# Optimization experiments

Hardware: AMD Instinct MI355X
Metric: run time of the kernel (lower is better)

## Reference

```python
import jax, jax.numpy as jnp
import numpy as np

C_CLIP = 10.0


def setup_inputs() -> dict:
    key = jax.random.key(0)
    ks = jax.random.split(key, 5)
    B, S, E, H = 128, 2048, 512, 512
    query = jax.random.normal(ks[0], (B, E), dtype=jnp.float32)
    target = jax.random.normal(ks[1], (B, S, E), dtype=jnp.float32)
    mask = jax.random.randint(ks[2], (B, S), 0, 2, dtype=jnp.int32)
    # torch.nn.Linear weights: [out, in], applied as x @ W.T + b
    Wq = jax.random.normal(ks[3], (H, E), dtype=jnp.float32) / np.sqrt(E)
    bq = jnp.zeros((H,), dtype=jnp.float32)
    Wk = jax.random.normal(ks[4], (H, E), dtype=jnp.float32) / np.sqrt(E)
    bk = jnp.zeros((H,), dtype=jnp.float32)
    return {"query": query, "target": target, "mask": mask,
            "Wq": Wq, "bq": bq, "Wk": Wk, "bk": bk}


def reference(query, target, mask, Wq, bq, Wk, bk):
    # q = W_q(query): [B, H]; k = W_k(target): [B, S, H]
    q = query @ Wq.T + bq
    k = jnp.einsum('bse,he->bsh', target, Wk) + bk
    # score qk[b,s] = sum_h q[b,h] * k[b,s,h]
    qk = jnp.einsum('bh,bsh->bs', q, k)
    qk = C_CLIP * jnp.tanh(qk)
    qk = jnp.where(mask == 1, -jnp.inf, qk)
    alpha = jax.nn.softmax(qk, axis=-1)
    return alpha
```

## Files before the change

### kernel.cpp

```cpp
#include <hip/hip_runtime.h>
#include <math.h>

#define Bsz 128
#define Ssz 2048
#define Esz 512
#define Hsz 512
#define C_CLIPF 10.0f
#define CHUNK 128

__device__ __forceinline__ float wave_reduce_sum(float p) {
    #pragma unroll
    for (int o = 32; o > 0; o >>= 1) p += __shfl_down(p, o);
    return p;
}

__device__ __forceinline__ float wave_reduce_max(float p) {
    #pragma unroll
    for (int o = 32; o > 0; o >>= 1) p = fmaxf(p, __shfl_down(p, o));
    return p;
}

__global__ __launch_bounds__(512) void k_qv(
    const float* __restrict__ query, const float* __restrict__ Wq,
    const float* __restrict__ bq, const float* __restrict__ Wk,
    const float* __restrict__ bk, float* __restrict__ v, float* __restrict__ c)
{
    const int b = blockIdx.x;
    const int tid = threadIdx.x;
    const int wave = tid >> 6, lane = tid & 63;
    __shared__ float q[Hsz];
    __shared__ float cpart[8];

    const float4* qp = (const float4*)(query + (size_t)b * Esz);
    const float4 qy0 = qp[lane * 2], qy1 = qp[lane * 2 + 1];

    for (int h = wave; h < Hsz; h += 8) {
        const float4* wr = (const float4*)(Wq + (size_t)h * Esz);
        const float4 a0 = wr[lane * 2], a1 = wr[lane * 2 + 1];
        float p = a0.x*qy0.x + a0.y*qy0.y + a0.z*qy0.z + a0.w*qy0.w
                + a1.x*qy1.x + a1.y*qy1.y + a1.z*qy1.z + a1.w*qy1.w;
        p = wave_reduce_sum(p);
        if (lane == 0) q[h] = p + bq[h];
    }
    __syncthreads();

    {
        float p = q[tid] * bk[tid];
        p = wave_reduce_sum(p);
        if (lane == 0) cpart[wave] = p;
    }
    __syncthreads();
    if (tid == 0) {
        float s = 0.f;
        #pragma unroll
        for (int w = 0; w < 8; ++w) s += cpart[w];
        c[b] = s;
    }

    float acc = 0.f;
    #pragma unroll 4
    for (int h = 0; h < Hsz; ++h) acc += q[h] * Wk[(size_t)h * Esz + tid];
    v[(size_t)b * Esz + tid] = acc;
}

__global__ __launch_bounds__(256) void k_score(
    const float* __restrict__ target, const int* __restrict__ mask,
    const float* __restrict__ v, const float* __restrict__ c,
    float* __restrict__ scores)
{
    const int nchunk = Ssz / CHUNK;
    const int b = blockIdx.x / nchunk;
    const int s0 = (blockIdx.x % nchunk) * CHUNK;
    const int wave = threadIdx.x >> 6, lane = threadIdx.x & 63;

    const float4* vp = (const float4*)(v + (size_t)b * Esz);
    const float4 v0 = vp[lane * 2], v1 = vp[lane * 2 + 1];
    const float cb = c[b];

    for (int r = wave; r < CHUNK; r += 4) {
        const int s = s0 + r;
        const float4* tp = (const float4*)(target + ((size_t)b * Ssz + s) * Esz);
        const float4 t0 = tp[lane * 2], t1 = tp[lane * 2 + 1];
        float p = t0.x*v0.x + t0.y*v0.y + t0.z*v0.z + t0.w*v0.w
                + t1.x*v1.x + t1.y*v1.y + t1.z*v1.z + t1.w*v1.w;
        p = wave_reduce_sum(p);
        if (lane == 0) {
            float sc;
            if (mask[(size_t)b * Ssz + s] == 1) sc = -INFINITY;
            else sc = C_CLIPF * tanhf(p + cb);
            scores[(size_t)b * Ssz + s] = sc;
        }
    }
}

__global__ __launch_bounds__(256) void k_softmax(float* __restrict__ out)
{
    const int b = blockIdx.x;
    const int tid = threadIdx.x;
    const int wave = tid >> 6, lane = tid & 63;
    __shared__ float red[4];

    float4* op = (float4*)(out + (size_t)b * Ssz);
    const float4 a0 = op[tid * 2], a1 = op[tid * 2 + 1];

    float m = fmaxf(fmaxf(fmaxf(a0.x, a0.y), fmaxf(a0.z, a0.w)),
                    fmaxf(fmaxf(a1.x, a1.y), fmaxf(a1.z, a1.w)));
    m = wave_reduce_max(m);
    if (lane == 0) red[wave] = m;
    __syncthreads();
    const float M = fmaxf(fmaxf(red[0], red[1]), fmaxf(red[2], red[3]));
    __syncthreads();

    float e0 = expf(a0.x - M), e1 = expf(a0.y - M), e2 = expf(a0.z - M), e3 = expf(a0.w - M);
    float e4 = expf(a1.x - M), e5 = expf(a1.y - M), e6 = expf(a1.z - M), e7 = expf(a1.w - M);

    float s = ((e0 + e1) + (e2 + e3)) + ((e4 + e5) + (e6 + e7));
    s = wave_reduce_sum(s);
    if (lane == 0) red[wave] = s;
    __syncthreads();
    const float SUM = ((red[0] + red[1]) + (red[2] + red[3]));
    const float inv = 1.0f / SUM;

    op[tid * 2]     = make_float4(e0 * inv, e1 * inv, e2 * inv, e3 * inv);
    op[tid * 2 + 1] = make_float4(e4 * inv, e5 * inv, e6 * inv, e7 * inv);
}

extern "C" void kernel_launch(void* const* d_in, const int* in_sizes, int n_in,
                              void* d_out, int out_size, void* d_ws, size_t ws_size,
                              hipStream_t stream) {
    const float* query  = (const float*)d_in[0];
    const float* target = (const float*)d_in[1];
    const int*   mask   = (const int*)d_in[2];
    const float* Wq     = (const float*)d_in[3];
    const float* bq     = (const float*)d_in[4];
    const float* Wk     = (const float*)d_in[5];
    const float* bk     = (const float*)d_in[6];
    float* out = (float*)d_out;

    float* v = (float*)d_ws;
    float* c = v + (size_t)Bsz * Esz;

    hipLaunchKernelGGL(k_qv, dim3(Bsz), dim3(512), 0, stream,
                       query, Wq, bq, Wk, bk, v, c);
    hipLaunchKernelGGL(k_score, dim3(Bsz * (Ssz / CHUNK)), dim3(256), 0, stream,
                       target, mask, v, c, out);
    hipLaunchKernelGGL(k_softmax, dim3(Bsz), dim3(256), 0, stream, out);
}
```

Before: 791.4 us.

## Batch row loads in score kernel with transpose-reduce; move tanh/mask into softmax

The score kernel now has each wave issue loads for 8 target rows at once and reduces them together with a butterfly merge of shuffles. Each lane ends up with one row's sum, so only 8 lanes write per group instead of one serial reduction per row. The bias add, tanh clip and mask are moved into the softmax kernel, which reads the mask vectorised and uses an exp2-based tanh. This aims to raise memory-level parallelism on the dominant streaming read of target, at the cost of more registers. CHUNK doubles and the unroll in k_qv grows.

```diff
diff --git a/kernel.cpp b/kernel.cpp
--- a/kernel.cpp
+++ b/kernel.cpp
@@ -6,7 +6,9 @@
 #define Esz 512
 #define Hsz 512
 #define C_CLIPF 10.0f
-#define CHUNK 128
+#define CHUNK 256
+#define NCHUNK (Ssz / CHUNK)
+#define NBLK (Bsz * NCHUNK)
 
 __device__ __forceinline__ float wave_reduce_sum(float p) {
     #pragma unroll
@@ -18,6 +20,12 @@
     #pragma unroll
     for (int o = 32; o > 0; o >>= 1) p = fmaxf(p, __shfl_down(p, o));
     return p;
+}
+
+__device__ __forceinline__ float merge_step(float a, float b, int xmask, int sel) {
+    float keep = sel ? b : a;
+    float send = sel ? a : b;
+    return keep + __shfl_xor(send, xmask);
 }
 
 __global__ __launch_bounds__(512) void k_qv(
@@ -58,71 +66,101 @@
     }
 
     float acc = 0.f;
-    #pragma unroll 4
+    #pragma unroll 8
     for (int h = 0; h < Hsz; ++h) acc += q[h] * Wk[(size_t)h * Esz + tid];
     v[(size_t)b * Esz + tid] = acc;
 }
 
 __global__ __launch_bounds__(256) void k_score(
-    const float* __restrict__ target, const int* __restrict__ mask,
-    const float* __restrict__ v, const float* __restrict__ c,
+    const float* __restrict__ target,
+    const float* __restrict__ v,
     float* __restrict__ scores)
 {
-    const int nchunk = Ssz / CHUNK;
-    const int b = blockIdx.x / nchunk;
-    const int s0 = (blockIdx.x % nchunk) * CHUNK;
+    const int b = blockIdx.x / NCHUNK;
+    const int s0 = (blockIdx.x % NCHUNK) * CHUNK;
     const int wave = threadIdx.x >> 6, lane = threadIdx.x & 63;
 
     const float4* vp = (const float4*)(v + (size_t)b * Esz);
     const float4 v0 = vp[lane * 2], v1 = vp[lane * 2 + 1];
-    const float cb = c[b];
 
-    for (int r = wave; r < CHUNK; r += 4) {
-        const int s = s0 + r;
-        const float4* tp = (const float4*)(target + ((size_t)b * Ssz + s) * Esz);
-        const float4 t0 = tp[lane * 2], t1 = tp[lane * 2 + 1];
-        float p = t0.x*v0.x + t0.y*v0.y + t0.z*v0.z + t0.w*v0.w
-                + t1.x*v1.x + t1.y*v1.y + t1.z*v1.z + t1.w*v1.w;
-        p = wave_reduce_sum(p);
-        if (lane == 0) {
-            float sc;
-            if (mask[(size_t)b * Ssz + s] == 1) sc = -INFINITY;
-            else sc = C_CLIPF * tanhf(p + cb);
-            scores[(size_t)b * Ssz + s] = sc;
+    const int rbase = s0 + wave * 64;
+    const float4* tp = (const float4*)(target + ((size_t)b * Ssz + rbase) * Esz);
+    float* op = scores + (size_t)b * Ssz + rbase;
+
+    for (int it = 0; it < 8; ++it) {
+        const float4* tpi = tp + (size_t)it * 8 * 128;
+        float4 ta[8], tb[8];
+        #pragma unroll
+        for (int i = 0; i < 8; ++i) {
+            ta[i] = tpi[i * 128 + lane * 2];
+            tb[i] = tpi[i * 128 + lane * 2 + 1];
         }
+        float p[8];
+        #pragma unroll
+        for (int i = 0; i < 8; ++i) {
+            p[i] = ta[i].x*v0.x + ta[i].y*v0.y + ta[i].z*v0.z + ta[i].w*v0.w
+                 + tb[i].x*v1.x + tb[i].y*v1.y + tb[i].z*v1.z + tb[i].w*v1.w;
+        }
+        float q0 = merge_step(p[0], p[1], 1, lane & 1);
+        float q1 = merge_step(p[2], p[3], 1, lane & 1);
+        float q2 = merge_step(p[4], p[5], 1, lane & 1);
+        float q3 = merge_step(p[6], p[7], 1, lane & 1);
+        float r0 = merge_step(q0, q1, 2, lane & 2);
+        float r1 = merge_step(q2, q3, 2, lane & 2);
+        float s  = merge_step(r0, r1, 4, lane & 4);
+        s += __shfl_xor(s, 8);
+        s += __shfl_xor(s, 16);
+        s += __shfl_xor(s, 32);
+        if (lane < 8) op[it * 8 + lane] = s;
     }
 }
 
-__global__ __launch_bounds__(256) void k_softmax(float* __restrict__ out)
+__global__ __launch_bounds__(256) void k_softmax(
+    const int* __restrict__ mask, const float* __restrict__ c,
+    float* __restrict__ out)
 {
     const int b = blockIdx.x;
     const int tid = threadIdx.x;
     const int wave = tid >> 6, lane = tid & 63;
     __shared__ float red[4];
 
+    const float cb = c[b];
     float4* op = (float4*)(out + (size_t)b * Ssz);
+    const int4* mp = (const int4*)(mask + (size_t)b * Ssz);
+
     const float4 a0 = op[tid * 2], a1 = op[tid * 2 + 1];
+    const int4  m0 = mp[tid * 2], m1 = mp[tid * 2 + 1];
 
-    float m = fmaxf(fmaxf(fmaxf(a0.x, a0.y), fmaxf(a0.z, a0.w)),
-                    fmaxf(fmaxf(a1.x, a1.y), fmaxf(a1.z, a1.w)));
+    float x[8] = {a0.x, a0.y, a0.z, a0.w, a1.x, a1.y, a1.z, a1.w};
+    const int mm[8] = {m0.x, m0.y, m0.z, m0.w, m1.x, m1.y, m1.z, m1.w};
+
+    #pragma unroll
+    for (int i = 0; i < 8; ++i) {
+        const float y = x[i] + cb;
+        const float t = 1.0f - 2.0f / (exp2f(y * 2.88539008177793f) + 1.0f);
+        x[i] = (mm[i] == 1) ? -INFINITY : C_CLIPF * t;
+    }
+
+    float m = x[0];
+    #pragma unroll
+    for (int i = 1; i < 8; ++i) m = fmaxf(m, x[i]);
     m = wave_reduce_max(m);
     if (lane == 0) red[wave] = m;
     __syncthreads();
     const float M = fmaxf(fmaxf(red[0], red[1]), fmaxf(red[2], red[3]));
     __syncthreads();
 
-    float e0 = expf(a0.x - M), e1 = expf(a0.y - M), e2 = expf(a0.z - M), e3 = expf(a0.w - M);
-    float e4 = expf(a1.x - M), e5 = expf(a1.y - M), e6 = expf(a1.z - M), e7 = expf(a1.w - M);
-
-    float s = ((e0 + e1) + (e2 + e3)) + ((e4 + e5) + (e6 + e7));
+    float e[8];
+    float s = 0.f;
+    #pragma unroll
+    for (int i = 0; i < 8; ++i) { e[i] = expf(x[i] - M); s += e[i]; }
     s = wave_reduce_sum(s);
     if (lane == 0) red[wave] = s;
     __syncthreads();
-    const float SUM = ((red[0] + red[1]) + (red[2] + red[3]));
-    const float inv = 1.0f / SUM;
+    const float inv = 1.0f / (((red[0] + red[1]) + (red[2] + red[3])));
 
-    op[tid * 2]     = make_float4(e0 * inv, e1 * inv, e2 * inv, e3 * inv);
-    op[tid * 2 + 1] = make_float4(e4 * inv, e5 * inv, e6 * inv, e7 * inv);
+    op[tid * 2]     = make_float4(e[0]*inv, e[1]*inv, e[2]*inv, e[3]*inv);
+    op[tid * 2 + 1] = make_float4(e[4]*inv, e[5]*inv, e[6]*inv, e[7]*inv);
 }
 
 extern "C" void kernel_launch(void* const* d_in, const int* in_sizes, int n_in,
@@ -142,7 +180,8 @@
 
     hipLaunchKernelGGL(k_qv, dim3(Bsz), dim3(512), 0, stream,
                        query, Wq, bq, Wk, bk, v, c);
-    hipLaunchKernelGGL(k_score, dim3(Bsz * (Ssz / CHUNK)), dim3(256), 0, stream,
-                       target, mask, v, c, out);
-    hipLaunchKernelGGL(k_softmax, dim3(Bsz), dim3(256), 0, stream, out);
+    hipLaunchKernelGGL(k_score, dim3(NBLK), dim3(256), 0, stream,
+                       target, v, out);
+    hipLaunchKernelGGL(k_softmax, dim3(Bsz), dim3(256), 0, stream,
+                       mask, c, out);
 }
```

After: 789.3 us. About the same (-0.3%).
